# Kernel tuning notes

Measured on AMD Instinct MI355X. Metric: run time of the kernel, lower is better.

The kernel has to match this reference:

```python
import jax, jax.numpy as jnp
import numpy as np

D_MODEL = 1024
N_HEADS = 16
HEAD_DIM = D_MODEL // N_HEADS
WINDOW = 512


def _rope(q, k, seq_len, head_dim):
    # interleaved RoPE, identical to the torch implementation
    theta = 1.0 / 10000.0 ** (jnp.arange(0, head_dim, 2, dtype=jnp.float32) / head_dim)
    pos = jnp.arange(seq_len, dtype=jnp.float32)
    freqs = jnp.outer(pos, theta)                      # [S, hD/2]
    cos_f = jnp.cos(freqs)[None, None]                 # [1,1,S,hD/2]
    sin_f = jnp.sin(freqs)[None, None]

    def rotate(x):
        x1, x2 = x[..., ::2], x[..., 1::2]
        return jnp.stack([x1 * cos_f - x2 * sin_f, x1 * sin_f + x2 * cos_f], axis=-1).reshape(x.shape)

    return rotate(q), rotate(k)


def _sliding_window_attn(q, k, v, W, scale):
    # chunked O(S*W) causal sliding-window attention
    B, nH, S, hD = q.shape
    n_chunks = (S + W - 1) // W
    pad_s = n_chunks * W - S
    k_pad = jnp.pad(k, ((0, 0), (0, 0), (W, pad_s), (0, 0)))
    v_pad = jnp.pad(v, ((0, 0), (0, 0), (W, pad_s), (0, 0)))
    q_pad = jnp.pad(q, ((0, 0), (0, 0), (0, pad_s), (0, 0)))
    q_c = q_pad.reshape(B, nH, n_chunks, W, hD)
    k_r = k_pad.reshape(B, nH, n_chunks + 1, W, hD)
    v_r = v_pad.reshape(B, nH, n_chunks + 1, W, hD)
    # window i = chunks [i, i+1] of the left-padded sequence (== torch unfold)
    k_c = jnp.concatenate([k_r[:, :, :-1], k_r[:, :, 1:]], axis=3)  # [B,nH,C,2W,hD]
    v_c = jnp.concatenate([v_r[:, :, :-1], v_r[:, :, 1:]], axis=3)
    attn = jnp.einsum('bhcqd,bhckd->bhcqk', q_c, k_c) * scale

    qi = jnp.arange(W)[:, None]
    ki = jnp.arange(2 * W)[None, :]
    cw_mask = (ki <= qi) | (ki > qi + W)               # [W, 2W]
    chunk_idx = jnp.arange(n_chunks)[:, None]
    abs_k = chunk_idx * W + ki - W                     # [C, 2W]
    pad_mask = (abs_k < 0) | (abs_k >= S)
    q_pos = jnp.arange(n_chunks * W).reshape(n_chunks, W)
    full_mask = cw_mask[None] | pad_mask[:, None, :] | (q_pos >= S)[..., None]  # [C,W,2W]

    attn = jnp.where(full_mask[None, None], -jnp.inf, attn)
    attn = jax.nn.softmax(attn, axis=-1)
    attn = jnp.nan_to_num(attn, nan=0.0)
    out = jnp.einsum('bhcqk,bhckd->bhcqd', attn, v_c)
    return out.reshape(B, nH, n_chunks * W, hD)[:, :, :S]


def _rmsnorm(x, w):
    eps = jnp.finfo(x.dtype).eps
    return x * jax.lax.rsqrt(jnp.mean(x * x, axis=-1, keepdims=True) + eps) * w


def _sdpa(q, k, v, scale):
    s = jnp.einsum('bhqd,bhkd->bhqk', q, k) * scale
    return jnp.einsum('bhqk,bhkd->bhqd', jax.nn.softmax(s, axis=-1), v)


def setup_inputs() -> dict:
    key = jax.random.key(0)
    ks = jax.random.split(key, 11)
    D = D_MODEL
    std = 0.02
    return {
        'x': jax.random.normal(ks[0], (2, 4096, D), jnp.float32),
        'landmarks': jax.random.normal(ks[1], (2, 256, D), jnp.float32),
        'archived_landmarks': jax.random.normal(ks[2], (2, 128, D), jnp.float32),
        'W_qkv': jax.random.normal(ks[3], (D, 3 * D), jnp.float32) * std,
        'W_lm': jax.random.normal(ks[4], (D, 2 * D), jnp.float32) * std,
        'W_arch': jax.random.normal(ks[5], (D, 2 * D), jnp.float32) * std,
        'W_o': jax.random.normal(ks[6], (D, D), jnp.float32) * std,
        'W_gate': jax.random.normal(ks[7], (3 * D, 2 * D), jnp.float32) * std,
        'g_local': jnp.ones((D,), jnp.float32),
        'g_lm': jnp.ones((D,), jnp.float32),
        'g_arch': jnp.ones((D,), jnp.float32),
    }


def reference(x, landmarks, archived_landmarks, W_qkv, W_lm, W_arch, W_o, W_gate, g_local, g_lm, g_arch):
    B, S, D = x.shape
    nH, hD = N_HEADS, HEAD_DIM
    scale = hD ** -0.5

    def rsh(t, L):
        return jnp.transpose(t.reshape(B, L, nH, hD), (0, 2, 1, 3))

    q, k, v = jnp.split(x @ W_qkv, 3, axis=-1)
    Q, K, V = rsh(q, S), rsh(k, S), rsh(v, S)
    Q, K = _rope(Q, K, S, hD)

    Weff = min(WINDOW, S)
    out_loc = _sliding_window_attn(Q, K, V, Weff, scale)  # S > Weff -> chunked path
    out_loc = _rmsnorm(jnp.transpose(out_loc, (0, 2, 1, 3)).reshape(B, S, D), g_local)

    L = landmarks.shape[1]
    K_lm, V_lm = jnp.split(landmarks @ W_lm, 2, axis=-1)
    out_lm = _sdpa(Q, rsh(K_lm, L), rsh(V_lm, L), scale)
    out_lm = _rmsnorm(jnp.transpose(out_lm, (0, 2, 1, 3)).reshape(B, S, D), g_lm)

    A = archived_landmarks.shape[1]
    K_a, V_a = jnp.split(archived_landmarks @ W_arch, 2, axis=-1)
    out_a = _sdpa(Q, rsh(K_a, A), rsh(V_a, A), scale)
    out_a = _rmsnorm(jnp.transpose(out_a, (0, 2, 1, 3)).reshape(B, S, D), g_arch)

    concat = jnp.concatenate([out_loc, out_lm, out_a], axis=-1)
    gate, value = jnp.split(concat @ W_gate, 2, axis=-1)
    return (jax.nn.silu(gate) * value) @ W_o
```

## Files before the change

kernel.cpp:

```cpp
#include <hip/hip_runtime.h>
#include <cstdint>
#include <cstddef>

typedef __bf16 bf16;
typedef __bf16 bf16x2 __attribute__((ext_vector_type(2)));
typedef __bf16 bf16x4 __attribute__((ext_vector_type(4)));
typedef __bf16 bf16x8 __attribute__((ext_vector_type(8)));
typedef float  f32x2 __attribute__((ext_vector_type(2)));
typedef float  f32x4 __attribute__((ext_vector_type(4)));

#define DEVFN __device__ __forceinline__
#define BAR()  asm volatile("s_barrier" ::: "memory")
#define VMW0() asm volatile("s_waitcnt vmcnt(0)" ::: "memory")
#define VMW3() asm volatile("s_waitcnt vmcnt(3)" ::: "memory")
#define VMW4() asm volatile("s_waitcnt vmcnt(4)" ::: "memory")
#define MFMA16 __builtin_amdgcn_mfma_f32_16x16x32_bf16

DEVFN void gld_lds16(void* lds, const void* g) {
  __builtin_amdgcn_global_load_lds(
      (__attribute__((address_space(1))) void*)g,
      (__attribute__((address_space(3))) void*)lds,
      16, 0, 0);
}

__global__ void cast_f32_bf16(const float* __restrict__ in, bf16* __restrict__ out, int n4) {
  int i = blockIdx.x * blockDim.x + threadIdx.x;
  if (i < n4) {
    f32x4 v = reinterpret_cast<const f32x4*>(in)[i];
    bf16x4 o;
    o[0] = (bf16)v[0]; o[1] = (bf16)v[1]; o[2] = (bf16)v[2]; o[3] = (bf16)v[3];
    reinterpret_cast<bf16x4*>(out)[i] = o;
  }
}

__global__ void transpose_cast(const float* __restrict__ in, bf16* __restrict__ out,
                               int R, int C) {
  __shared__ float t[32][33];
  int tx = threadIdx.x, ty = threadIdx.y;
  int c = blockIdx.x * 32 + tx;
  #pragma unroll
  for (int j = 0; j < 4; ++j) {
    int r = blockIdx.y * 32 + ty + j * 8;
    t[ty + j * 8][tx] = in[(size_t)r * C + c];
  }
  __syncthreads();
  int rr = blockIdx.y * 32 + tx;
  #pragma unroll
  for (int j = 0; j < 4; ++j) {
    int cc = blockIdx.x * 32 + ty + j * 8;
    out[(size_t)cc * R + rr] = (bf16)t[tx][ty + j * 8];
  }
}

__global__ void rope_table(float* __restrict__ tab) {
  int idx = blockIdx.x * 256 + threadIdx.x;
  int s = idx >> 5, i = idx & 31;
  float theta = powf(10000.f, -(float)(2 * i) * (1.f / 64.f));
  float f = (float)s * theta;
  tab[idx * 2]     = cosf(f);
  tab[idx * 2 + 1] = sinf(f);
}

template<typename OT>
__global__ __launch_bounds__(512) void gemm256(
    const bf16* __restrict__ A, const bf16* __restrict__ Bt, OT* __restrict__ C,
    int M, int N, int K) {
  __shared__ alignas(16) bf16 lds[2][2][2][256 * 32];
  const int tid = threadIdx.x;
  const int w = tid >> 6, l = tid & 63;
  const int l15 = l & 15, lg = l >> 4;
  const int wm = w >> 2, wn = w & 3;
  const int nwg = gridDim.x, qx = nwg >> 3;
  const int swz = (blockIdx.x & 7) * qx + (blockIdx.x >> 3);
  const int gx = N >> 8;
  const int m0 = (swz / gx) << 8;
  const int n0 = (swz % gx) << 8;
  const int nt = K >> 6;

  auto stage = [&](int b, int ab, int kk, int t) {
    const bf16* __restrict__ src = ab ? Bt : A;
    const int base0 = ab ? n0 : m0;
    const int k0 = (t << 6) + (kk << 5);
    #pragma unroll
    for (int i = 0; i < 2; ++i) {
      int u = i * 512 + tid;
      int row = u >> 2, slot = u & 3;
      int sslot = slot ^ ((row >> 1) & 3);
      gld_lds16(&lds[b][ab][kk][(i * 512 + w * 64) * 8],
                src + (size_t)(base0 + row) * K + k0 + sslot * 8);
    }
  };
  auto rd = [&](int b, int ab, int kk, int r) -> bf16x8 {
    return *reinterpret_cast<const bf16x8*>(
        &lds[b][ab][kk][(r << 5) + ((lg ^ ((r >> 1) & 3)) << 3)]);
  };

  f32x4 acc[8][4] = {};
  bf16x8 aLo[4], aHi[4], bfr[4];

  stage(0, 0, 0, 0);
  stage(0, 1, 0, 0);
  stage(0, 0, 1, 0);
  stage(0, 1, 1, 0);
  VMW4();
  BAR();

  for (int t = 0; t < nt; ++t) {
    const int c = t & 1;
    const bool st = (t + 1) < nt;
    #pragma unroll
    for (int f = 0; f < 4; ++f) aLo[f] = rd(c, 0, 0, wm * 128 + f * 16 + l15);
    #pragma unroll
    for (int f = 0; f < 4; ++f) bfr[f] = rd(c, 1, 0, wn * 64 + f * 16 + l15);
    if (st) stage(c ^ 1, 0, 0, t + 1);
    BAR();
    __builtin_amdgcn_s_setprio(1);
    #pragma unroll
    for (int mi = 0; mi < 4; ++mi)
      #pragma unroll
      for (int ni = 0; ni < 4; ++ni)
        acc[mi][ni] = MFMA16(aLo[mi], bfr[ni], acc[mi][ni], 0, 0, 0);
    __builtin_amdgcn_s_setprio(0);
    #pragma unroll
    for (int f = 0; f < 4; ++f) aHi[f] = rd(c, 0, 0, wm * 128 + (f + 4) * 16 + l15);
    BAR();
    if (st) stage(c ^ 1, 1, 0, t + 1);
    BAR();
    __builtin_amdgcn_s_setprio(1);
    #pragma unroll
    for (int mi = 0; mi < 4; ++mi)
      #pragma unroll
      for (int ni = 0; ni < 4; ++ni)
        acc[mi + 4][ni] = MFMA16(aHi[mi], bfr[ni], acc[mi + 4][ni], 0, 0, 0);
    __builtin_amdgcn_s_setprio(0);
    if (st) { VMW4(); } else { VMW0(); }
    BAR();
    #pragma unroll
    for (int f = 0; f < 4; ++f) aLo[f] = rd(c, 0, 1, wm * 128 + f * 16 + l15);
    #pragma unroll
    for (int f = 0; f < 4; ++f) bfr[f] = rd(c, 1, 1, wn * 64 + f * 16 + l15);
    if (st) stage(c ^ 1, 0, 1, t + 1);
    BAR();
    __builtin_amdgcn_s_setprio(1);
    #pragma unroll
    for (int mi = 0; mi < 4; ++mi)
      #pragma unroll
      for (int ni = 0; ni < 4; ++ni)
        acc[mi][ni] = MFMA16(aLo[mi], bfr[ni], acc[mi][ni], 0, 0, 0);
    __builtin_amdgcn_s_setprio(0);
    #pragma unroll
    for (int f = 0; f < 4; ++f) aHi[f] = rd(c, 0, 1, wm * 128 + (f + 4) * 16 + l15);
    BAR();
    if (st) stage(c ^ 1, 1, 1, t + 1);
    BAR();
    __builtin_amdgcn_s_setprio(1);
    #pragma unroll
    for (int mi = 0; mi < 4; ++mi)
      #pragma unroll
      for (int ni = 0; ni < 4; ++ni)
        acc[mi + 4][ni] = MFMA16(aHi[mi], bfr[ni], acc[mi + 4][ni], 0, 0, 0);
    __builtin_amdgcn_s_setprio(0);
    VMW4();
    BAR();
  }

  #pragma unroll
  for (int mi = 0; mi < 8; ++mi) {
    #pragma unroll
    for (int r = 0; r < 4; ++r) {
      int row = m0 + wm * 128 + mi * 16 + lg * 4 + r;
      OT* crow = C + (size_t)row * N + n0 + wn * 64 + l15;
      #pragma unroll
      for (int ni = 0; ni < 4; ++ni) crow[ni * 16] = (OT)acc[mi][ni][r];
    }
  }
}

template<typename OT>
__global__ __launch_bounds__(512) void gemm256n128(
    const bf16* __restrict__ A, const bf16* __restrict__ Bt, OT* __restrict__ C,
    int M, int N, int K) {
  __shared__ alignas(16) bf16 ldsA[2][2][256 * 32];
  __shared__ alignas(16) bf16 ldsB[2][2][128 * 32];
  const int tid = threadIdx.x;
  const int w = tid >> 6, l = tid & 63;
  const int l15 = l & 15, lg = l >> 4;
  const int wm = w >> 1, wn = w & 1;
  const int nwg = gridDim.x, qx = nwg >> 3;
  const int swz = (blockIdx.x & 7) * qx + (blockIdx.x >> 3);
  const int gx = N >> 7;
  const int m0 = (swz / gx) << 8;
  const int n0 = (swz % gx) << 7;
  const int nt = K >> 6;

  auto stageA = [&](int b, int kk, int t) {
    const int k0 = (t << 6) + (kk << 5);
    #pragma unroll
    for (int i = 0; i < 2; ++i) {
      int u = i * 512 + tid;
      int row = u >> 2, slot = u & 3;
      int ss = slot ^ ((row >> 1) & 3);
      gld_lds16(&ldsA[b][kk][(i * 512 + w * 64) * 8],
                A + (size_t)(m0 + row) * K + k0 + ss * 8);
    }
  };
  auto stageB = [&](int b, int kk, int t) {
    const int k0 = (t << 6) + (kk << 5);
    int row = tid >> 2, slot = tid & 3;
    int ss = slot ^ ((row >> 1) & 3);
    gld_lds16(&ldsB[b][kk][(w * 64) * 8],
              Bt + (size_t)(n0 + row) * K + k0 + ss * 8);
  };
  auto rdA = [&](int b, int kk, int r) -> bf16x8 {
    return *reinterpret_cast<const bf16x8*>(
        &ldsA[b][kk][(r << 5) + ((lg ^ ((r >> 1) & 3)) << 3)]);
  };
  auto rdB = [&](int b, int kk, int r) -> bf16x8 {
    return *reinterpret_cast<const bf16x8*>(
        &ldsB[b][kk][(r << 5) + ((lg ^ ((r >> 1) & 3)) << 3)]);
  };

  f32x4 acc[4][4] = {};
  bf16x8 af[4], bf[4];

  stageA(0, 0, 0); stageB(0, 0, 0);
  stageA(0, 1, 0); stageB(0, 1, 0);
  VMW3();
  BAR();

  for (int t = 0; t < nt; ++t) {
    const int c = t & 1;
    const bool st = (t + 1) < nt;
    #pragma unroll
    for (int kk = 0; kk < 2; ++kk) {
      #pragma unroll
      for (int f = 0; f < 4; ++f) af[f] = rdA(c, kk, wm * 64 + f * 16 + l15);
      #pragma unroll
      for (int f = 0; f < 4; ++f) bf[f] = rdB(c, kk, wn * 64 + f * 16 + l15);
      if (st) { stageA(c ^ 1, kk, t + 1); stageB(c ^ 1, kk, t + 1); }
      BAR();
      __builtin_amdgcn_s_setprio(1);
      #pragma unroll
      for (int mi = 0; mi < 4; ++mi)
        #pragma unroll
        for (int ni = 0; ni < 4; ++ni)
          acc[mi][ni] = MFMA16(af[mi], bf[ni], acc[mi][ni], 0, 0, 0);
      __builtin_amdgcn_s_setprio(0);
      if (st) { VMW3(); }
      else if (kk == 0) { VMW0(); }
      BAR();
    }
  }

  #pragma unroll
  for (int mi = 0; mi < 4; ++mi) {
    #pragma unroll
    for (int r = 0; r < 4; ++r) {
      int row = m0 + wm * 64 + mi * 16 + lg * 4 + r;
      OT* crow = C + (size_t)row * N + n0 + wn * 64 + l15;
      #pragma unroll
      for (int ni = 0; ni < 4; ++ni) crow[ni * 16] = (OT)acc[mi][ni][r];
    }
  }
}

template<typename OT>
__global__ __launch_bounds__(256) void gemm_bf16(
    const bf16* __restrict__ A, const bf16* __restrict__ Bt, OT* __restrict__ C,
    int M, int N, int K) {
  __shared__ alignas(16) bf16 As[128 * 64];
  __shared__ alignas(16) bf16 Bs[128 * 64];
  int tid = threadIdx.x;
  int w = tid >> 6, l = tid & 63;
  int l15 = l & 15, lg = l >> 4;
  int m0 = blockIdx.y * 128;
  int n0 = blockIdx.x * 128;
  int wr = (w >> 1) * 64, wc = (w & 1) * 64;
  f32x4 acc[4][4] = {};
  const size_t aBase = (size_t)m0 * K;
  const size_t bBase = (size_t)n0 * K;
  int nk = K >> 6;
  for (int kt = 0; kt < nk; ++kt) {
    int k0 = kt << 6;
    #pragma unroll
    for (int it = 0; it < 4; ++it) {
      int c = it * 256 + tid;
      int row = c >> 3, c8 = c & 7;
      gld_lds16(&As[(size_t)(it * 256 + w * 64) * 8],
                A + aBase + (size_t)row * K + k0 + c8 * 8);
      gld_lds16(&Bs[(size_t)(it * 256 + w * 64) * 8],
                Bt + bBase + (size_t)row * K + k0 + c8 * 8);
    }
    __syncthreads();
    #pragma unroll
    for (int kk = 0; kk < 64; kk += 32) {
      bf16x8 a[4], b[4];
      #pragma unroll
      for (int i = 0; i < 4; ++i)
        a[i] = *reinterpret_cast<const bf16x8*>(&As[(wr + i * 16 + l15) * 64 + kk + lg * 8]);
      #pragma unroll
      for (int i = 0; i < 4; ++i)
        b[i] = *reinterpret_cast<const bf16x8*>(&Bs[(wc + i * 16 + l15) * 64 + kk + lg * 8]);
      #pragma unroll
      for (int mi = 0; mi < 4; ++mi)
        #pragma unroll
        for (int ni = 0; ni < 4; ++ni)
          acc[mi][ni] = MFMA16(a[mi], b[ni], acc[mi][ni], 0, 0, 0);
    }
    __syncthreads();
  }
  #pragma unroll
  for (int mi = 0; mi < 4; ++mi) {
    #pragma unroll
    for (int r = 0; r < 4; ++r) {
      int row = m0 + wr + mi * 16 + lg * 4 + r;
      OT* crow = C + (size_t)row * N + n0 + wc + l15;
      #pragma unroll
      for (int ni = 0; ni < 4; ++ni) crow[ni * 16] = (OT)acc[mi][ni][r];
    }
  }
}

__global__ void rope_qk(const bf16* __restrict__ qkv, const float* __restrict__ tab,
                        bf16* __restrict__ Qb, bf16* __restrict__ Kb) {
  int idx = blockIdx.x * 256 + threadIdx.x;
  int i = idx & 31;
  int h = (idx >> 5) & 15;
  int bs = idx >> 9;
  int s = bs & 4095;
  int b = bs >> 12;
  const bf16* row = qkv + (size_t)bs * 3072;
  bf16x2 q2 = *reinterpret_cast<const bf16x2*>(row + h * 64 + 2 * i);
  bf16x2 k2 = *reinterpret_cast<const bf16x2*>(row + 1024 + h * 64 + 2 * i);
  f32x2 cs = *reinterpret_cast<const f32x2*>(tab + s * 64 + 2 * i);
  float c = cs[0], sn = cs[1];
  float q0 = (float)q2[0], q1 = (float)q2[1];
  float k0 = (float)k2[0], k1 = (float)k2[1];
  size_t ob = (((size_t)(b * 16 + h) * 4096) + s) * 64 + 2 * i;
  bf16x2 qo, ko;
  qo[0] = (bf16)((q0 * c - q1 * sn) * 0.125f);
  qo[1] = (bf16)((q0 * sn + q1 * c) * 0.125f);
  ko[0] = (bf16)(k0 * c - k1 * sn);
  ko[1] = (bf16)(k0 * sn + k1 * c);
  *reinterpret_cast<bf16x2*>(Qb + ob) = qo;
  *reinterpret_cast<bf16x2*>(Kb + ob) = ko;
}

__global__ void kv_post(const bf16* __restrict__ kv, bf16* __restrict__ Kdst,
                        bf16* __restrict__ Vt, int Lk, int rs, int koff, int voff) {
  __shared__ float t[64][65];
  int s0 = blockIdx.x * 64;
  int h = blockIdx.y, b = blockIdx.z;
  int tid = threadIdx.x;
  int lane_d = tid & 63;
  int rq = tid >> 6;
  const bf16* base = kv + (size_t)b * Lk * rs;
  if (Kdst) {
    #pragma unroll
    for (int r = 0; r < 16; ++r) {
      int si = r * 4 + rq;
      Kdst[(((size_t)(b * 16 + h) * Lk) + s0 + si) * 64 + lane_d] =
          base[(size_t)(s0 + si) * rs + koff + h * 64 + lane_d];
    }
  }
  #pragma unroll
  for (int r = 0; r < 16; ++r) {
    int si = r * 4 + rq;
    t[si][lane_d] = (float)base[(size_t)(s0 + si) * rs + voff + h * 64 + lane_d];
  }
  __syncthreads();
  #pragma unroll
  for (int r = 0; r < 16; ++r) {
    int d = r * 4 + rq;
    Vt[(((size_t)(b * 16 + h) * 64) + d) * Lk + s0 + lane_d] = (bf16)t[lane_d][d];
  }
}

__global__ __launch_bounds__(256) void attn_win(
    const bf16* __restrict__ Qb, const bf16* __restrict__ Kb,
    const bf16* __restrict__ Vt, bf16* __restrict__ outc) {
  constexpr int S = 4096;
  __shared__ alignas(16) bf16 Ks[2][64 * 64];
  __shared__ alignas(16) bf16 Vs[2][64 * 64];
  __shared__ alignas(16) bf16 Ps[4][2][16 * 72];
  const int tid = threadIdx.x;
  const int w = tid >> 6, l = tid & 63;
  const int l15 = l & 15, lg = l >> 4;
  const int h = blockIdx.y, b = blockIdx.z;
  const int Q0 = blockIdx.x * 128;
  const int qt0 = Q0 >> 6;

  const bf16* Kbase = Kb + ((size_t)(b * 16 + h) * S) * 64;
  const bf16* Vbase = Vt + ((size_t)(b * 16 + h) * 64) * S;

  bf16x8 qf[2][2];
  #pragma unroll
  for (int c = 0; c < 2; ++c) {
    size_t qrow = (((size_t)(b * 16 + h) * S) + Q0 + w * 32 + c * 16 + l15) * 64;
    qf[c][0] = *reinterpret_cast<const bf16x8*>(Qb + qrow + lg * 8);
    qf[c][1] = *reinterpret_cast<const bf16x8*>(Qb + qrow + 32 + lg * 8);
  }

  const int kt_hi = qt0 + 1;
  const int kt_lo = qt0 >= 8 ? qt0 - 8 : 0;

  auto stage = [&](int buf, int kt) {
    const bf16* kg = Kbase + (size_t)kt * 64 * 64;
    #pragma unroll
    for (int it = 0; it < 2; ++it) {
      int u = it * 256 + tid;
      int row = u >> 3, sl = u & 7;
      gld_lds16(&Ks[buf][(it * 256 + w * 64) * 8], kg + row * 64 + (sl ^ (row & 7)) * 8);
    }
    #pragma unroll
    for (int it = 0; it < 2; ++it) {
      int u = it * 256 + tid;
      int row = u >> 3, sl = u & 7;
      gld_lds16(&Vs[buf][(it * 256 + w * 64) * 8],
                Vbase + (size_t)row * S + kt * 64 + (sl ^ (row & 7)) * 8);
    }
  };

  float mrow[2] = {-30000.f, -30000.f}, lsum[2] = {0.f, 0.f};
  f32x4 acc[2][4] = {};

  stage(0, kt_hi);

  int i = 0;
  for (int kt = kt_hi; kt >= kt_lo; --kt, ++i) {
    const int buf = i & 1;
    if (kt > kt_lo) { stage(buf ^ 1, kt - 1); VMW4(); } else { VMW0(); }
    BAR();

    f32x4 st[2][4] = {};
    #pragma unroll
    for (int kk = 0; kk < 2; ++kk) {
      #pragma unroll
      for (int f = 0; f < 4; ++f) {
        bf16x8 kf = *reinterpret_cast<const bf16x8*>(
            &Ks[buf][(f * 16 + l15) * 64 + (((kk * 4 + lg) ^ (l15 & 7)) << 3)]);
        #pragma unroll
        for (int c = 0; c < 2; ++c)
          st[c][f] = MFMA16(kf, qf[c][kk], st[c][f], 0, 0, 0);
      }
    }

    if (kt >= qt0) {
      #pragma unroll
      for (int c = 0; c < 2; ++c) {
        int q = Q0 + w * 32 + c * 16 + l15;
        #pragma unroll
        for (int f = 0; f < 4; ++f)
          #pragma unroll
          for (int r = 0; r < 4; ++r)
            if (kt * 64 + f * 16 + lg * 4 + r > q) st[c][f][r] = -1e30f;
      }
    }
    if (kt <= qt0 - 7) {
      #pragma unroll
      for (int c = 0; c < 2; ++c) {
        int q = Q0 + w * 32 + c * 16 + l15;
        #pragma unroll
        for (int f = 0; f < 4; ++f)
          #pragma unroll
          for (int r = 0; r < 4; ++r)
            if (kt * 64 + f * 16 + lg * 4 + r <= q - 512) st[c][f][r] = -1e30f;
      }
    }

    #pragma unroll
    for (int c = 0; c < 2; ++c) {
      float rm = -1e30f;
      #pragma unroll
      for (int f = 0; f < 4; ++f)
        #pragma unroll
        for (int r = 0; r < 4; ++r) rm = fmaxf(rm, st[c][f][r]);
      rm = fmaxf(rm, __shfl_xor(rm, 16));
      rm = fmaxf(rm, __shfl_xor(rm, 32));
      float mnew = fmaxf(mrow[c], rm);
      float fsc = __expf(mrow[c] - mnew);
      float ps = 0.f;
      #pragma unroll
      for (int f = 0; f < 4; ++f) {
        bf16x4 pv;
        #pragma unroll
        for (int r = 0; r < 4; ++r) {
          float p = __expf(st[c][f][r] - mnew);
          ps += p;
          pv[r] = (bf16)p;
        }
        *reinterpret_cast<bf16x4*>(&Ps[w][c][l15 * 72 + f * 16 + lg * 4]) = pv;
      }
      ps += __shfl_xor(ps, 16);
      ps += __shfl_xor(ps, 32);
      lsum[c] = lsum[c] * fsc + ps;
      mrow[c] = mnew;
      #pragma unroll
      for (int r = 0; r < 4; ++r) {
        float fr = __shfl(fsc, lg * 4 + r);
        #pragma unroll
        for (int f = 0; f < 4; ++f) acc[c][f][r] *= fr;
      }
    }

    #pragma unroll
    for (int kk = 0; kk < 2; ++kk) {
      bf16x8 pa[2];
      #pragma unroll
      for (int c = 0; c < 2; ++c)
        pa[c] = *reinterpret_cast<const bf16x8*>(&Ps[w][c][l15 * 72 + kk * 32 + lg * 8]);
      #pragma unroll
      for (int f = 0; f < 4; ++f) {
        bf16x8 vf = *reinterpret_cast<const bf16x8*>(
            &Vs[buf][(f * 16 + l15) * 64 + (((kk * 4 + lg) ^ (l15 & 7)) << 3)]);
        #pragma unroll
        for (int c = 0; c < 2; ++c)
          acc[c][f] = MFMA16(pa[c], vf, acc[c][f], 0, 0, 0);
      }
    }
    BAR();
  }

  #pragma unroll
  for (int c = 0; c < 2; ++c) {
    float inv = 1.f / lsum[c];
    #pragma unroll
    for (int r = 0; r < 4; ++r) {
      float ir = __shfl(inv, lg * 4 + r);
      int srow = Q0 + w * 32 + c * 16 + lg * 4 + r;
      bf16* orow = outc + ((size_t)b * S + srow) * 3072 + h * 64 + l15;
      #pragma unroll
      for (int f = 0; f < 4; ++f) orow[f * 16] = (bf16)(acc[c][f][r] * ir);
    }
  }
}

template<int LKV, int NQI>
__global__ __launch_bounds__(512) void attn_res(
    const bf16* __restrict__ Qb, const bf16* __restrict__ Kb,
    const bf16* __restrict__ Vt, bf16* __restrict__ outc, int col_off) {
  constexpr int S = 4096;
  __shared__ alignas(16) bf16 Ks[LKV * 64];
  __shared__ alignas(16) bf16 Vs[64 * LKV];
  __shared__ alignas(16) bf16 Ps[8][2][16 * 72];
  const int tid = threadIdx.x;
  const int w = tid >> 6, l = tid & 63;
  const int l15 = l & 15, lg = l >> 4;
  const int h = blockIdx.y, b = blockIdx.z;
  const bf16* Kg = Kb + ((size_t)(b * 16 + h) * LKV) * 64;
  const bf16* Vg = Vt + ((size_t)(b * 16 + h) * 64) * LKV;

  constexpr int NU = LKV / 64;
  constexpr int SPR = LKV / 8;
  #pragma unroll
  for (int i = 0; i < NU; ++i) {
    int u = i * 512 + tid;
    int row = u >> 3, sl = u & 7;
    gld_lds16(&Ks[(i * 512 + w * 64) * 8], Kg + row * 64 + (sl ^ (row & 7)) * 8);
  }
  #pragma unroll
  for (int i = 0; i < NU; ++i) {
    int u = i * 512 + tid;
    int row = u / SPR, sl = u % SPR;
    gld_lds16(&Vs[(i * 512 + w * 64) * 8],
              Vg + (size_t)row * LKV + ((sl & ~7) + ((sl & 7) ^ (row & 7))) * 8);
  }
  __syncthreads();

  for (int qi = 0; qi < NQI; ++qi) {
    const int Q0 = (blockIdx.x * NQI + qi) * 256 + w * 32;
    bf16x8 qf[2][2];
    #pragma unroll
    for (int c = 0; c < 2; ++c) {
      size_t qrow = (((size_t)(b * 16 + h) * S) + Q0 + c * 16 + l15) * 64;
      qf[c][0] = *reinterpret_cast<const bf16x8*>(Qb + qrow + lg * 8);
      qf[c][1] = *reinterpret_cast<const bf16x8*>(Qb + qrow + 32 + lg * 8);
    }
    float mrow[2] = {-30000.f, -30000.f}, lsum[2] = {0.f, 0.f};
    f32x4 acc[2][4] = {};

    #pragma unroll
    for (int kt = 0; kt < LKV / 64; ++kt) {
      f32x4 st[2][4] = {};
      #pragma unroll
      for (int kk = 0; kk < 2; ++kk) {
        #pragma unroll
        for (int f = 0; f < 4; ++f) {
          bf16x8 kf = *reinterpret_cast<const bf16x8*>(
              &Ks[(kt * 64 + f * 16 + l15) * 64 + (((kk * 4 + lg) ^ (l15 & 7)) << 3)]);
          #pragma unroll
          for (int c = 0; c < 2; ++c)
            st[c][f] = MFMA16(kf, qf[c][kk], st[c][f], 0, 0, 0);
        }
      }
      #pragma unroll
      for (int c = 0; c < 2; ++c) {
        float rm = -1e30f;
        #pragma unroll
        for (int f = 0; f < 4; ++f)
          #pragma unroll
          for (int r = 0; r < 4; ++r) rm = fmaxf(rm, st[c][f][r]);
        rm = fmaxf(rm, __shfl_xor(rm, 16));
        rm = fmaxf(rm, __shfl_xor(rm, 32));
        float mnew = fmaxf(mrow[c], rm);
        float fsc = __expf(mrow[c] - mnew);
        float ps = 0.f;
        #pragma unroll
        for (int f = 0; f < 4; ++f) {
          bf16x4 pv;
          #pragma unroll
          for (int r = 0; r < 4; ++r) {
            float p = __expf(st[c][f][r] - mnew);
            ps += p;
            pv[r] = (bf16)p;
          }
          *reinterpret_cast<bf16x4*>(&Ps[w][c][l15 * 72 + f * 16 + lg * 4]) = pv;
        }
        ps += __shfl_xor(ps, 16);
        ps += __shfl_xor(ps, 32);
        lsum[c] = lsum[c] * fsc + ps;
        mrow[c] = mnew;
        #pragma unroll
        for (int r = 0; r < 4; ++r) {
          float fr = __shfl(fsc, lg * 4 + r);
          #pragma unroll
          for (int f = 0; f < 4; ++f) acc[c][f][r] *= fr;
        }
      }
      #pragma unroll
      for (int kk = 0; kk < 2; ++kk) {
        bf16x8 pa[2];
        #pragma unroll
        for (int c = 0; c < 2; ++c)
          pa[c] = *reinterpret_cast<const bf16x8*>(&Ps[w][c][l15 * 72 + kk * 32 + lg * 8]);
        #pragma unroll
        for (int f = 0; f < 4; ++f) {
          bf16x8 vf = *reinterpret_cast<const bf16x8*>(
              &Vs[(f * 16 + l15) * LKV + ((kt * 8 + ((kk * 4 + lg) ^ (l15 & 7))) << 3)]);
          #pragma unroll
          for (int c = 0; c < 2; ++c)
            acc[c][f] = MFMA16(pa[c], vf, acc[c][f], 0, 0, 0);
        }
      }
    }

    #pragma unroll
    for (int c = 0; c < 2; ++c) {
      float inv = 1.f / lsum[c];
      #pragma unroll
      for (int r = 0; r < 4; ++r) {
        float ir = __shfl(inv, lg * 4 + r);
        int srow = Q0 + c * 16 + lg * 4 + r;
        bf16* orow = outc + ((size_t)b * S + srow) * 3072 + col_off + h * 64 + l15;
        #pragma unroll
        for (int f = 0; f < 4; ++f) orow[f * 16] = (bf16)(acc[c][f][r] * ir);
      }
    }
  }
}

__global__ __launch_bounds__(256) void rmsnorm_kernel(
    bf16* data, const float* __restrict__ g0,
    const float* __restrict__ g1, const float* __restrict__ g2) {
  int token = blockIdx.x;
  int seg = blockIdx.y;
  const float* g = seg == 0 ? g0 : (seg == 1 ? g1 : g2);
  int tid = threadIdx.x;
  size_t base = (size_t)token * 3072 + seg * 1024;
  bf16x4 bv = reinterpret_cast<const bf16x4*>(data + base)[tid];
  f32x4 v;
  #pragma unroll
  for (int j = 0; j < 4; ++j) v[j] = (float)bv[j];
  float ss = v[0] * v[0] + v[1] * v[1] + v[2] * v[2] + v[3] * v[3];
  #pragma unroll
  for (int m = 1; m < 64; m <<= 1) ss += __shfl_xor(ss, m);
  __shared__ float red[4];
  if ((tid & 63) == 0) red[tid >> 6] = ss;
  __syncthreads();
  float tot = red[0] + red[1] + red[2] + red[3];
  float sc = rsqrtf(tot * (1.f / 1024.f) + 1.19209290e-07f);
  f32x4 gv = reinterpret_cast<const f32x4*>(g)[tid];
  bf16x4 o;
  #pragma unroll
  for (int j = 0; j < 4; ++j) o[j] = (bf16)(v[j] * sc * gv[j]);
  reinterpret_cast<bf16x4*>(data + base)[tid] = o;
}

__global__ void silu_kernel(const bf16* __restrict__ gv, bf16* __restrict__ out) {
  int T = blockIdx.x * 256 + threadIdx.x;
  int row = T >> 8, c4 = (T & 255) * 4;
  bf16x4 g = *reinterpret_cast<const bf16x4*>(gv + (size_t)row * 2048 + c4);
  bf16x4 vv = *reinterpret_cast<const bf16x4*>(gv + (size_t)row * 2048 + 1024 + c4);
  bf16x4 o;
  #pragma unroll
  for (int j = 0; j < 4; ++j) {
    float x = (float)g[j];
    o[j] = (bf16)((x / (1.f + __expf(-x))) * (float)vv[j]);
  }
  *reinterpret_cast<bf16x4*>(out + (size_t)row * 1024 + c4) = o;
}

extern "C" void kernel_launch(void* const* d_in, const int* in_sizes, int n_in,
                              void* d_out, int out_size, void* d_ws, size_t ws_size,
                              hipStream_t stream) {
  (void)in_sizes; (void)n_in; (void)out_size; (void)ws_size;
  const float* x       = (const float*)d_in[0];
  const float* lm      = (const float*)d_in[1];
  const float* arch    = (const float*)d_in[2];
  const float* W_qkv   = (const float*)d_in[3];
  const float* W_lm    = (const float*)d_in[4];
  const float* W_arch  = (const float*)d_in[5];
  const float* W_o     = (const float*)d_in[6];
  const float* W_gate  = (const float*)d_in[7];
  const float* g_local = (const float*)d_in[8];
  const float* g_lm    = (const float*)d_in[9];
  const float* g_arch  = (const float*)d_in[10];
  float* out = (float*)d_out;

  char* ws = (char*)d_ws;
  size_t off = 0;
  auto alloc = [&](size_t bytes) -> void* {
    void* p = ws + off;
    off += (bytes + 255) & ~(size_t)255;
    return p;
  };
  bf16*  Wqkv_t   = (bf16*) alloc(3072ull * 1024 * 2);
  bf16*  Wlm_t    = (bf16*) alloc(2048ull * 1024 * 2);
  bf16*  Warch_t  = (bf16*) alloc(2048ull * 1024 * 2);
  bf16*  Wgate_t  = (bf16*) alloc(2048ull * 3072 * 2);
  bf16*  Wo_t     = (bf16*) alloc(1024ull * 1024 * 2);
  bf16*  lm_bf    = (bf16*) alloc(512ull * 1024 * 2);
  bf16*  arch_bf  = (bf16*) alloc(256ull * 1024 * 2);
  float* ropetab  = (float*)alloc(4096ull * 64 * 4);
  bf16*  Klm      = (bf16*) alloc(2ull * 16 * 256 * 64 * 2);
  bf16*  Vlm_t    = (bf16*) alloc(2ull * 16 * 64 * 256 * 2);
  bf16*  Ka       = (bf16*) alloc(2ull * 16 * 128 * 64 * 2);
  bf16*  Va_t     = (bf16*) alloc(2ull * 16 * 64 * 128 * 2);
  bf16*  lmkv_bf  = (bf16*) alloc(512ull * 2048 * 2);
  bf16*  akv_bf   = (bf16*) alloc(256ull * 2048 * 2);
  char* R1 = (char*)alloc(8192ull * 1024 * 2);
  bf16* x_bf  = (bf16*)R1;
  bf16* gated = (bf16*)R1;
  char* R2 = (char*)alloc(8192ull * 3072 * 2);
  bf16* qkv_bf  = (bf16*)R2;
  bf16* concatb = (bf16*)R2;
  char* R3 = (char*)alloc(3ull * 16 * 1024 * 1024);
  bf16* Qb = (bf16*)R3;
  bf16* Kb = (bf16*)(R3 + 16ull * 1024 * 1024);
  bf16* Vt = (bf16*)(R3 + 32ull * 1024 * 1024);
  bf16* gv = (bf16*)R3;

  transpose_cast<<<dim3(96, 32), dim3(32, 8), 0, stream>>>(W_qkv, Wqkv_t, 1024, 3072);
  transpose_cast<<<dim3(64, 32), dim3(32, 8), 0, stream>>>(W_lm, Wlm_t, 1024, 2048);
  transpose_cast<<<dim3(64, 32), dim3(32, 8), 0, stream>>>(W_arch, Warch_t, 1024, 2048);
  transpose_cast<<<dim3(64, 96), dim3(32, 8), 0, stream>>>(W_gate, Wgate_t, 3072, 2048);
  transpose_cast<<<dim3(32, 32), dim3(32, 8), 0, stream>>>(W_o, Wo_t, 1024, 1024);
  cast_f32_bf16<<<8192, 256, 0, stream>>>(x, x_bf, 8192 * 1024 / 4);
  cast_f32_bf16<<<512, 256, 0, stream>>>(lm, lm_bf, 512 * 1024 / 4);
  cast_f32_bf16<<<256, 256, 0, stream>>>(arch, arch_bf, 256 * 1024 / 4);
  rope_table<<<512, 256, 0, stream>>>(ropetab);

  gemm256n128<bf16><<<32 * 24, 512, 0, stream>>>(x_bf, Wqkv_t, qkv_bf, 8192, 3072, 1024);
  gemm_bf16<bf16><<<dim3(16, 4), 256, 0, stream>>>(lm_bf, Wlm_t, lmkv_bf, 512, 2048, 1024);
  gemm_bf16<bf16><<<dim3(16, 2), 256, 0, stream>>>(arch_bf, Warch_t, akv_bf, 256, 2048, 1024);

  rope_qk<<<16384, 256, 0, stream>>>(qkv_bf, ropetab, Qb, Kb);
  kv_post<<<dim3(64, 16, 2), 256, 0, stream>>>(qkv_bf, nullptr, Vt, 4096, 3072, 0, 2048);
  kv_post<<<dim3(4, 16, 2), 256, 0, stream>>>(lmkv_bf, Klm, Vlm_t, 256, 2048, 0, 1024);
  kv_post<<<dim3(2, 16, 2), 256, 0, stream>>>(akv_bf, Ka, Va_t, 128, 2048, 0, 1024);

  attn_win<<<dim3(32, 16, 2), 256, 0, stream>>>(Qb, Kb, Vt, concatb);
  attn_res<256, 2><<<dim3(8, 16, 2), 512, 0, stream>>>(Qb, Klm, Vlm_t, concatb, 1024);
  attn_res<128, 2><<<dim3(8, 16, 2), 512, 0, stream>>>(Qb, Ka, Va_t, concatb, 2048);

  rmsnorm_kernel<<<dim3(8192, 3), 256, 0, stream>>>(concatb, g_local, g_lm, g_arch);

  gemm256<bf16><<<32 * 8, 512, 0, stream>>>(concatb, Wgate_t, gv, 8192, 2048, 3072);
  silu_kernel<<<8192, 256, 0, stream>>>(gv, gated);
  gemm256n128<float><<<32 * 8, 512, 0, stream>>>(gated, Wo_t, out, 8192, 1024, 1024);
}
```

Before: 448.0 us.

## Fuse SiLU gating into gate GEMM, split-K landmark GEMMs, 64-row attention tiles

The gate GEMM now loads interleaved gate and value column blocks so that each tile holds matching gate and value columns. It applies SiLU times value in its epilogue, which removes the separate silu kernel and the intermediate gv round trip through memory. The small landmark and archive projections use split-K over 4 slices into fp32 partial buffers, summed inside a new kv_post4, to raise parallelism for these tiny GEMMs. The sliding-window attention kernel is also changed from 128-query blocks to 64-query blocks, doubling the grid but halving reuse of each loaded K/V tile.

```diff
diff --git a/kernel.cpp b/kernel.cpp
--- a/kernel.cpp
+++ b/kernel.cpp
@@ -61,10 +61,9 @@
   tab[idx * 2 + 1] = sinf(f);
 }
 
-template<typename OT>
-__global__ __launch_bounds__(512) void gemm256(
-    const bf16* __restrict__ A, const bf16* __restrict__ Bt, OT* __restrict__ C,
-    int M, int N, int K) {
+__global__ __launch_bounds__(512) void gemm_gate4(
+    const bf16* __restrict__ A, const bf16* __restrict__ Bt,
+    bf16* __restrict__ G, int K) {
   __shared__ alignas(16) bf16 lds[2][2][2][256 * 32];
   const int tid = threadIdx.x;
   const int w = tid >> 6, l = tid & 63;
@@ -72,22 +71,27 @@
   const int wm = w >> 2, wn = w & 3;
   const int nwg = gridDim.x, qx = nwg >> 3;
   const int swz = (blockIdx.x & 7) * qx + (blockIdx.x >> 3);
-  const int gx = N >> 8;
-  const int m0 = (swz / gx) << 8;
-  const int n0 = (swz % gx) << 8;
+  const int m0 = (swz >> 3) << 8;
+  const int n0 = (swz & 7) << 7;
   const int nt = K >> 6;
 
   auto stage = [&](int b, int ab, int kk, int t) {
-    const bf16* __restrict__ src = ab ? Bt : A;
-    const int base0 = ab ? n0 : m0;
     const int k0 = (t << 6) + (kk << 5);
     #pragma unroll
     for (int i = 0; i < 2; ++i) {
       int u = i * 512 + tid;
       int row = u >> 2, slot = u & 3;
-      int sslot = slot ^ ((row >> 1) & 3);
+      int ss = slot ^ ((row >> 1) & 3);
+      int grow;
+      if (ab) {
+        int q = row >> 6, o = row & 63;
+        grow = (o < 32) ? (n0 + q * 32 + o) : (1024 + n0 + q * 32 + o - 32);
+      } else {
+        grow = m0 + row;
+      }
+      const bf16* src = ab ? Bt : A;
       gld_lds16(&lds[b][ab][kk][(i * 512 + w * 64) * 8],
-                src + (size_t)(base0 + row) * K + k0 + sslot * 8);
+                src + (size_t)grow * K + k0 + ss * 8);
     }
   };
   auto rd = [&](int b, int ab, int kk, int r) -> bf16x8 {
@@ -169,9 +173,12 @@
     #pragma unroll
     for (int r = 0; r < 4; ++r) {
       int row = m0 + wm * 128 + mi * 16 + lg * 4 + r;
-      OT* crow = C + (size_t)row * N + n0 + wn * 64 + l15;
-      #pragma unroll
-      for (int ni = 0; ni < 4; ++ni) crow[ni * 16] = (OT)acc[mi][ni][r];
+      bf16* grow = G + (size_t)row * 1024 + n0 + wn * 32 + l15;
+      #pragma unroll
+      for (int ni = 0; ni < 2; ++ni) {
+        float g = acc[mi][ni][r], v = acc[mi][ni + 2][r];
+        grow[ni * 16] = (bf16)((g / (1.f + __expf(-g))) * v);
+      }
     }
   }
 }
@@ -264,10 +271,9 @@
   }
 }
 
-template<typename OT>
-__global__ __launch_bounds__(256) void gemm_bf16(
-    const bf16* __restrict__ A, const bf16* __restrict__ Bt, OT* __restrict__ C,
-    int M, int N, int K) {
+__global__ __launch_bounds__(256) void gemm_skt(
+    const bf16* __restrict__ A, const bf16* __restrict__ Bt, float* __restrict__ C,
+    int M, int N, int Ktot, int Kc) {
   __shared__ alignas(16) bf16 As[128 * 64];
   __shared__ alignas(16) bf16 Bs[128 * 64];
   int tid = threadIdx.x;
@@ -275,21 +281,22 @@
   int l15 = l & 15, lg = l >> 4;
   int m0 = blockIdx.y * 128;
   int n0 = blockIdx.x * 128;
+  int sk = blockIdx.z;
+  int kb = sk * Kc;
+  float* Cs = C + (size_t)sk * M * N;
   int wr = (w >> 1) * 64, wc = (w & 1) * 64;
   f32x4 acc[4][4] = {};
-  const size_t aBase = (size_t)m0 * K;
-  const size_t bBase = (size_t)n0 * K;
-  int nk = K >> 6;
+  int nk = Kc >> 6;
   for (int kt = 0; kt < nk; ++kt) {
-    int k0 = kt << 6;
+    int k0 = kb + (kt << 6);
     #pragma unroll
     for (int it = 0; it < 4; ++it) {
       int c = it * 256 + tid;
       int row = c >> 3, c8 = c & 7;
       gld_lds16(&As[(size_t)(it * 256 + w * 64) * 8],
-                A + aBase + (size_t)row * K + k0 + c8 * 8);
+                A + (size_t)(m0 + row) * Ktot + k0 + c8 * 8);
       gld_lds16(&Bs[(size_t)(it * 256 + w * 64) * 8],
-                Bt + bBase + (size_t)row * K + k0 + c8 * 8);
+                Bt + (size_t)(n0 + row) * Ktot + k0 + c8 * 8);
     }
     __syncthreads();
     #pragma unroll
@@ -314,9 +321,9 @@
     #pragma unroll
     for (int r = 0; r < 4; ++r) {
       int row = m0 + wr + mi * 16 + lg * 4 + r;
-      OT* crow = C + (size_t)row * N + n0 + wc + l15;
-      #pragma unroll
-      for (int ni = 0; ni < 4; ++ni) crow[ni * 16] = (OT)acc[mi][ni][r];
+      float* crow = Cs + (size_t)row * N + n0 + wc + l15;
+      #pragma unroll
+      for (int ni = 0; ni < 4; ++ni) crow[ni * 16] = acc[mi][ni][r];
     }
   }
 }
@@ -376,33 +383,58 @@
   }
 }
 
-__global__ __launch_bounds__(256) void attn_win(
+__global__ void kv_post4(const float* __restrict__ kv, bf16* __restrict__ Kdst,
+                         bf16* __restrict__ Vt, int Lk, int Mtot) {
+  __shared__ float t[64][65];
+  int s0 = blockIdx.x * 64;
+  int h = blockIdx.y, b = blockIdx.z;
+  int tid = threadIdx.x;
+  int lane_d = tid & 63;
+  int rq = tid >> 6;
+  const size_t slab = (size_t)Mtot * 2048;
+  const float* base = kv + (size_t)b * Lk * 2048;
+  #pragma unroll
+  for (int r = 0; r < 16; ++r) {
+    int si = r * 4 + rq;
+    size_t o = (size_t)(s0 + si) * 2048 + h * 64 + lane_d;
+    float kvv = base[o] + base[slab + o] + base[2 * slab + o] + base[3 * slab + o];
+    size_t ov = o + 1024;
+    float vvv = base[ov] + base[slab + ov] + base[2 * slab + ov] + base[3 * slab + ov];
+    Kdst[(((size_t)(b * 16 + h) * Lk) + s0 + si) * 64 + lane_d] = (bf16)kvv;
+    t[si][lane_d] = vvv;
+  }
+  __syncthreads();
+  #pragma unroll
+  for (int r = 0; r < 16; ++r) {
+    int d = r * 4 + rq;
+    Vt[(((size_t)(b * 16 + h) * 64) + d) * Lk + s0 + lane_d] = (bf16)t[lane_d][d];
+  }
+}
+
+__global__ __launch_bounds__(256) void attn64(
     const bf16* __restrict__ Qb, const bf16* __restrict__ Kb,
     const bf16* __restrict__ Vt, bf16* __restrict__ outc) {
   constexpr int S = 4096;
   __shared__ alignas(16) bf16 Ks[2][64 * 64];
   __shared__ alignas(16) bf16 Vs[2][64 * 64];
-  __shared__ alignas(16) bf16 Ps[4][2][16 * 72];
-  const int tid = threadIdx.x;
-  const int w = tid >> 6, l = tid & 63;
-  const int l15 = l & 15, lg = l >> 4;
-  const int h = blockIdx.y, b = blockIdx.z;
-  const int Q0 = blockIdx.x * 128;
-  const int qt0 = Q0 >> 6;
-
+  __shared__ alignas(16) bf16 Ps[4][16 * 72];
+  int tid = threadIdx.x;
+  int w = tid >> 6, l = tid & 63;
+  int l15 = l & 15, lg = l >> 4;
+  int qt = blockIdx.x, h = blockIdx.y, b = blockIdx.z;
+
+  size_t qrow = (((size_t)(b * 16 + h) * S) + qt * 64 + w * 16 + l15) * 64;
+  bf16x8 qf[2];
+  qf[0] = *reinterpret_cast<const bf16x8*>(Qb + qrow + lg * 8);
+  qf[1] = *reinterpret_cast<const bf16x8*>(Qb + qrow + 32 + lg * 8);
   const bf16* Kbase = Kb + ((size_t)(b * 16 + h) * S) * 64;
   const bf16* Vbase = Vt + ((size_t)(b * 16 + h) * 64) * S;
 
-  bf16x8 qf[2][2];
-  #pragma unroll
-  for (int c = 0; c < 2; ++c) {
-    size_t qrow = (((size_t)(b * 16 + h) * S) + Q0 + w * 32 + c * 16 + l15) * 64;
-    qf[c][0] = *reinterpret_cast<const bf16x8*>(Qb + qrow + lg * 8);
-    qf[c][1] = *reinterpret_cast<const bf16x8*>(Qb + qrow + 32 + lg * 8);
-  }
-
-  const int kt_hi = qt0 + 1;
-  const int kt_lo = qt0 >= 8 ? qt0 - 8 : 0;
+  float mrow = -1e30f, lsum = 0.f;
+  f32x4 acc[4] = {};
+
+  const int kt_hi = qt;
+  const int kt_lo = qt >= 8 ? qt - 8 : 0;
 
   auto stage = [&](int buf, int kt) {
     const bf16* kg = Kbase + (size_t)kt * 64 * 64;
@@ -421,9 +453,6 @@
     }
   };
 
-  float mrow[2] = {-30000.f, -30000.f}, lsum[2] = {0.f, 0.f};
-  f32x4 acc[2][4] = {};
-
   stage(0, kt_hi);
 
   int i = 0;
@@ -432,106 +461,86 @@
     if (kt > kt_lo) { stage(buf ^ 1, kt - 1); VMW4(); } else { VMW0(); }
     BAR();
 
-    f32x4 st[2][4] = {};
+    f32x4 st[4] = {};
     #pragma unroll
     for (int kk = 0; kk < 2; ++kk) {
       #pragma unroll
       for (int f = 0; f < 4; ++f) {
         bf16x8 kf = *reinterpret_cast<const bf16x8*>(
             &Ks[buf][(f * 16 + l15) * 64 + (((kk * 4 + lg) ^ (l15 & 7)) << 3)]);
-        #pragma unroll
-        for (int c = 0; c < 2; ++c)
-          st[c][f] = MFMA16(kf, qf[c][kk], st[c][f], 0, 0, 0);
-      }
-    }
-
-    if (kt >= qt0) {
-      #pragma unroll
-      for (int c = 0; c < 2; ++c) {
-        int q = Q0 + w * 32 + c * 16 + l15;
-        #pragma unroll
-        for (int f = 0; f < 4; ++f)
-          #pragma unroll
-          for (int r = 0; r < 4; ++r)
-            if (kt * 64 + f * 16 + lg * 4 + r > q) st[c][f][r] = -1e30f;
-      }
-    }
-    if (kt <= qt0 - 7) {
-      #pragma unroll
-      for (int c = 0; c < 2; ++c) {
-        int q = Q0 + w * 32 + c * 16 + l15;
-        #pragma unroll
-        for (int f = 0; f < 4; ++f)
-          #pragma unroll
-          for (int r = 0; r < 4; ++r)
-            if (kt * 64 + f * 16 + lg * 4 + r <= q - 512) st[c][f][r] = -1e30f;
-      }
-    }
-
-    #pragma unroll
-    for (int c = 0; c < 2; ++c) {
-      float rm = -1e30f;
+        st[f] = MFMA16(kf, qf[kk], st[f], 0, 0, 0);
+      }
+    }
+
+    int qi = w * 16 + l15;
+    if (kt == qt) {
       #pragma unroll
       for (int f = 0; f < 4; ++f)
         #pragma unroll
-        for (int r = 0; r < 4; ++r) rm = fmaxf(rm, st[c][f][r]);
-      rm = fmaxf(rm, __shfl_xor(rm, 16));
-      rm = fmaxf(rm, __shfl_xor(rm, 32));
-      float mnew = fmaxf(mrow[c], rm);
-      float fsc = __expf(mrow[c] - mnew);
-      float ps = 0.f;
-      #pragma unroll
-      for (int f = 0; f < 4; ++f) {
-        bf16x4 pv;
-        #pragma unroll
-        for (int r = 0; r < 4; ++r) {
-          float p = __expf(st[c][f][r] - mnew);
-          ps += p;
-          pv[r] = (bf16)p;
-        }
-        *reinterpret_cast<bf16x4*>(&Ps[w][c][l15 * 72 + f * 16 + lg * 4]) = pv;
-      }
-      ps += __shfl_xor(ps, 16);
-      ps += __shfl_xor(ps, 32);
-      lsum[c] = lsum[c] * fsc + ps;
-      mrow[c] = mnew;
+        for (int r = 0; r < 4; ++r)
+          if (f * 16 + lg * 4 + r > qi) st[f][r] = -1e30f;
+    } else if (kt == qt - 8) {
+      #pragma unroll
+      for (int f = 0; f < 4; ++f)
+        #pragma unroll
+        for (int r = 0; r < 4; ++r)
+          if (f * 16 + lg * 4 + r <= qi) st[f][r] = -1e30f;
+    }
+
+    float rm = -1e30f;
+    #pragma unroll
+    for (int f = 0; f < 4; ++f)
+      #pragma unroll
+      for (int r = 0; r < 4; ++r) rm = fmaxf(rm, st[f][r]);
+    rm = fmaxf(rm, __shfl_xor(rm, 16));
+    rm = fmaxf(rm, __shfl_xor(rm, 32));
+    float mnew = fmaxf(mrow, rm);
+    float fsc = __expf(mrow - mnew);
+    float ps = 0.f;
+    #pragma unroll
+    for (int f = 0; f < 4; ++f) {
+      bf16x4 pv;
       #pragma unroll
       for (int r = 0; r < 4; ++r) {
-        float fr = __shfl(fsc, lg * 4 + r);
-        #pragma unroll
-        for (int f = 0; f < 4; ++f) acc[c][f][r] *= fr;
-      }
+        float p = __expf(st[f][r] - mnew);
+        ps += p;
+        pv[r] = (bf16)p;
+      }
+      *reinterpret_cast<bf16x4*>(&Ps[w][l15 * 72 + f * 16 + lg * 4]) = pv;
+    }
+    ps += __shfl_xor(ps, 16);
+    ps += __shfl_xor(ps, 32);
+    lsum = lsum * fsc + ps;
+    mrow = mnew;
+
+    #pragma unroll
+    for (int r = 0; r < 4; ++r) {
+      float fr = __shfl(fsc, lg * 4 + r);
+      #pragma unroll
+      for (int f = 0; f < 4; ++f) acc[f][r] *= fr;
     }
 
     #pragma unroll
     for (int kk = 0; kk < 2; ++kk) {
-      bf16x8 pa[2];
-      #pragma unroll
-      for (int c = 0; c < 2; ++c)
-        pa[c] = *reinterpret_cast<const bf16x8*>(&Ps[w][c][l15 * 72 + kk * 32 + lg * 8]);
+      bf16x8 pa = *reinterpret_cast<const bf16x8*>(&Ps[w][l15 * 72 + kk * 32 + lg * 8]);
       #pragma unroll
       for (int f = 0; f < 4; ++f) {
         bf16x8 vf = *reinterpret_cast<const bf16x8*>(
             &Vs[buf][(f * 16 + l15) * 64 + (((kk * 4 + lg) ^ (l15 & 7)) << 3)]);
-        #pragma unroll
-        for (int c = 0; c < 2; ++c)
-          acc[c][f] = MFMA16(pa[c], vf, acc[c][f], 0, 0, 0);
-      }
-    }
-    BAR();
-  }
-
-  #pragma unroll
-  for (int c = 0; c < 2; ++c) {
-    float inv = 1.f / lsum[c];
-    #pragma unroll
-    for (int r = 0; r < 4; ++r) {
-      float ir = __shfl(inv, lg * 4 + r);
-      int srow = Q0 + w * 32 + c * 16 + lg * 4 + r;
-      bf16* orow = outc + ((size_t)b * S + srow) * 3072 + h * 64 + l15;
-      #pragma unroll
-      for (int f = 0; f < 4; ++f) orow[f * 16] = (bf16)(acc[c][f][r] * ir);
-    }
+        acc[f] = MFMA16(pa, vf, acc[f], 0, 0, 0);
+      }
+    }
+    BAR();
+  }
+
+  float inv = 1.f / lsum;
+  #pragma unroll
+  for (int r = 0; r < 4; ++r) {
+    float ir = __shfl(inv, lg * 4 + r);
+    int srow = qt * 64 + w * 16 + lg * 4 + r;
+    bf16* orow = outc + ((size_t)b * S + srow) * 3072 + h * 64 + l15;
+    #pragma unroll
+    for (int f = 0; f < 4; ++f) orow[f * 16] = (bf16)(acc[f][r] * ir);
   }
 }
 
@@ -684,20 +693,6 @@
   #pragma unroll
   for (int j = 0; j < 4; ++j) o[j] = (bf16)(v[j] * sc * gv[j]);
   reinterpret_cast<bf16x4*>(data + base)[tid] = o;
-}
-
-__global__ void silu_kernel(const bf16* __restrict__ gv, bf16* __restrict__ out) {
-  int T = blockIdx.x * 256 + threadIdx.x;
-  int row = T >> 8, c4 = (T & 255) * 4;
-  bf16x4 g = *reinterpret_cast<const bf16x4*>(gv + (size_t)row * 2048 + c4);
-  bf16x4 vv = *reinterpret_cast<const bf16x4*>(gv + (size_t)row * 2048 + 1024 + c4);
-  bf16x4 o;
-  #pragma unroll
-  for (int j = 0; j < 4; ++j) {
-    float x = (float)g[j];
-    o[j] = (bf16)((x / (1.f + __expf(-x))) * (float)vv[j]);
-  }
-  *reinterpret_cast<bf16x4*>(out + (size_t)row * 1024 + c4) = o;
 }
 
 extern "C" void kernel_launch(void* const* d_in, const int* in_sizes, int n_in,
@@ -736,11 +731,11 @@
   bf16*  Vlm_t    = (bf16*) alloc(2ull * 16 * 64 * 256 * 2);
   bf16*  Ka       = (bf16*) alloc(2ull * 16 * 128 * 64 * 2);
   bf16*  Va_t     = (bf16*) alloc(2ull * 16 * 64 * 128 * 2);
-  bf16*  lmkv_bf  = (bf16*) alloc(512ull * 2048 * 2);
-  bf16*  akv_bf   = (bf16*) alloc(256ull * 2048 * 2);
-  char* R1 = (char*)alloc(8192ull * 1024 * 2);
-  bf16* x_bf  = (bf16*)R1;
-  bf16* gated = (bf16*)R1;
+  char* R1 = (char*)alloc(24ull * 1024 * 1024);
+  bf16*  x_bf   = (bf16*)R1;
+  float* lmP    = (float*)R1;
+  float* archP  = (float*)(R1 + 16ull * 1024 * 1024);
+  bf16*  gated  = (bf16*)R1;
   char* R2 = (char*)alloc(8192ull * 3072 * 2);
   bf16* qkv_bf  = (bf16*)R2;
   bf16* concatb = (bf16*)R2;
@@ -748,7 +743,6 @@
   bf16* Qb = (bf16*)R3;
   bf16* Kb = (bf16*)(R3 + 16ull * 1024 * 1024);
   bf16* Vt = (bf16*)(R3 + 32ull * 1024 * 1024);
-  bf16* gv = (bf16*)R3;
 
   transpose_cast<<<dim3(96, 32), dim3(32, 8), 0, stream>>>(W_qkv, Wqkv_t, 1024, 3072);
   transpose_cast<<<dim3(64, 32), dim3(32, 8), 0, stream>>>(W_lm, Wlm_t, 1024, 2048);
@@ -760,22 +754,21 @@
   cast_f32_bf16<<<256, 256, 0, stream>>>(arch, arch_bf, 256 * 1024 / 4);
   rope_table<<<512, 256, 0, stream>>>(ropetab);
 
-  gemm256n128<bf16><<<32 * 24, 512, 0, stream>>>(x_bf, Wqkv_t, qkv_bf, 8192, 3072, 1024);
-  gemm_bf16<bf16><<<dim3(16, 4), 256, 0, stream>>>(lm_bf, Wlm_t, lmkv_bf, 512, 2048, 1024);
-  gemm_bf16<bf16><<<dim3(16, 2), 256, 0, stream>>>(arch_bf, Warch_t, akv_bf, 256, 2048, 1024);
+  gemm256n128<bf16><<<768, 512, 0, stream>>>(x_bf, Wqkv_t, qkv_bf, 8192, 3072, 1024);
+  gemm_skt<<<dim3(16, 4, 4), 256, 0, stream>>>(lm_bf, Wlm_t, lmP, 512, 2048, 1024, 256);
+  gemm_skt<<<dim3(16, 2, 4), 256, 0, stream>>>(arch_bf, Warch_t, archP, 256, 2048, 1024, 256);
 
   rope_qk<<<16384, 256, 0, stream>>>(qkv_bf, ropetab, Qb, Kb);
   kv_post<<<dim3(64, 16, 2), 256, 0, stream>>>(qkv_bf, nullptr, Vt, 4096, 3072, 0, 2048);
-  kv_post<<<dim3(4, 16, 2), 256, 0, stream>>>(lmkv_bf, Klm, Vlm_t, 256, 2048, 0, 1024);
-  kv_post<<<dim3(2, 16, 2), 256, 0, stream>>>(akv_bf, Ka, Va_t, 128, 2048, 0, 1024);
-
-  attn_win<<<dim3(32, 16, 2), 256, 0, stream>>>(Qb, Kb, Vt, concatb);
+  kv_post4<<<dim3(4, 16, 2), 256, 0, stream>>>(lmP, Klm, Vlm_t, 256, 512);
+  kv_post4<<<dim3(2, 16, 2), 256, 0, stream>>>(archP, Ka, Va_t, 128, 256);
+
+  attn64<<<dim3(64, 16, 2), 256, 0, stream>>>(Qb, Kb, Vt, concatb);
   attn_res<256, 2><<<dim3(8, 16, 2), 512, 0, stream>>>(Qb, Klm, Vlm_t, concatb, 1024);
   attn_res<128, 2><<<dim3(8, 16, 2), 512, 0, stream>>>(Qb, Ka, Va_t, concatb, 2048);
 
   rmsnorm_kernel<<<dim3(8192, 3), 256, 0, stream>>>(concatb, g_local, g_lm, g_arch);
 
-  gemm256<bf16><<<32 * 8, 512, 0, stream>>>(concatb, Wgate_t, gv, 8192, 2048, 3072);
-  silu_kernel<<<8192, 256, 0, stream>>>(gv, gated);
-  gemm256n128<float><<<32 * 8, 512, 0, stream>>>(gated, Wo_t, out, 8192, 1024, 1024);
-}
+  gemm_gate4<<<256, 512, 0, stream>>>(concatb, Wgate_t, gated, 3072);
+  gemm256n128<float><<<256, 512, 0, stream>>>(gated, Wo_t, out, 8192, 1024, 1024);
+}
```

Result: no change. 456.2 us (+1.8%).
